# Performance work log

Hardware: AMD Instinct MI355X
Metric: run time of the kernel (lower is better)

Reference implementation:

```python
import jax, jax.numpy as jnp
import numpy as np

N = 20000      # nodes
E = 320000     # edges
IN = 128       # in_channels
HID = 64       # hidden_channels (per-head out dim, concat=False -> mean over heads)
HEADS = 4
NEG_SLOPE = 0.2


def setup_inputs() -> dict:
    key = jax.random.key(0)
    ks = jax.random.split(key, 18)
    g = lambda i, shape: jax.random.normal(ks[i], shape, dtype=jnp.float32) * 0.05
    return {
        "x": jax.random.normal(ks[0], (N, IN), dtype=jnp.float32),
        "edge_index": jax.random.randint(ks[1], (2, E), 0, N),
        # GATConv params: lin weight (no bias in PyG lin), att_src/att_dst, out bias
        "W0": g(2, (IN, HEADS * HID)),
        "W1": g(3, (HID, HEADS * HID)),
        "W2": g(4, (HID, HEADS * HID)),
        "W3": g(5, (HID, HEADS * HID)),
        "a_src": g(6, (4, HEADS, HID)),
        "a_dst": g(7, (4, HEADS, HID)),
        "gat_b": g(8, (4, HID)),
        # residual projection for layer 0 (in_channels != hidden_channels)
        "res_W": g(9, (IN, HID)),
        "res_b": g(10, (HID,)),
        # edge classifier MLP: 2*HID -> HID -> HID -> 1
        "lin_W0": g(11, (2 * HID, HID)),
        "lin_b0": g(12, (HID,)),
        "lin_W1": g(13, (HID, HID)),
        "lin_b1": g(14, (HID,)),
        "lin_W2": g(15, (HID, 1)),
        "lin_b2": g(16, (1,)),
    }


def gat_conv(x, src, dst, W, asrc, adst, b, n):
    # x: [n, F_in]; src/dst: [E_tot] (self-loops included); W: [F_in, H*C]
    h = (x @ W).reshape(n, HEADS, HID)                     # [n, H, C]
    s_src = (h * asrc).sum(-1)                             # [n, H]
    s_dst = (h * adst).sum(-1)                             # [n, H]
    e = jax.nn.leaky_relu(s_src[src] + s_dst[dst], NEG_SLOPE)  # [E_tot, H]
    # segment softmax over incoming edges of each dst node
    m = jax.ops.segment_max(e, dst, num_segments=n)        # [n, H]
    p = jnp.exp(e - m[dst])
    z = jax.ops.segment_sum(p, dst, num_segments=n)
    alpha = p / z[dst]                                     # [E_tot, H]
    out = jax.ops.segment_sum(alpha[:, :, None] * h[src], dst, num_segments=n)  # [n, H, C]
    return out.mean(axis=1) + b                            # concat=False -> mean over heads


def reference(x, edge_index, W0, W1, W2, W3, a_src, a_dst, gat_b,
              res_W, res_b, lin_W0, lin_b0, lin_W1, lin_b1, lin_W2, lin_b2):
    n = x.shape[0]
    loop = jnp.arange(n)
    src = jnp.concatenate([edge_index[0], loop])  # PyG GATConv adds self-loops
    dst = jnp.concatenate([edge_index[1], loop])
    Ws = [W0, W1, W2, W3]
    h = x
    for i in range(4):
        h_prev = h
        h = gat_conv(h, src, dst, Ws[i], a_src[i], a_dst[i], gat_b[i], n)
        if i == 0:
            h = h + h_prev @ res_W + res_b   # projected residual
        else:
            h = h + h_prev
        h = jax.nn.elu(h)
    row, col = edge_index[0], edge_index[1]
    er = jnp.concatenate([h[row], h[col]], axis=1)        # [E, 2*HID]
    er = jax.nn.relu(er @ lin_W0 + lin_b0)                # shapes differ -> no residual
    er = jax.nn.relu(er @ lin_W1 + lin_b1 + er)           # shapes match -> residual
    logits = er @ lin_W2 + lin_b2                          # [E, 1]
    return logits
```

## Files before the change

### kernel.cpp

```cpp
#include <hip/hip_runtime.h>
#include <hip/hip_bf16.h>

#define NSLOPE 0.2f
#define MAXDEG 64

typedef short bf16x8 __attribute__((ext_vector_type(8)));
typedef float f32x4 __attribute__((ext_vector_type(4)));

__device__ __forceinline__ unsigned short f2b(float f) {
    unsigned u = __float_as_uint(f);
    unsigned r = (u + 0x7FFFu + ((u >> 16) & 1u)) >> 16;
    return (unsigned short)r;
}
__device__ __forceinline__ float b2f_lo(unsigned w) {
    return __uint_as_float(w << 16);
}
__device__ __forceinline__ float b2f_hi(unsigned w) {
    return __uint_as_float(w & 0xFFFF0000u);
}
__device__ __forceinline__ float b2f_s(short s) {
    return __uint_as_float(((unsigned)(unsigned short)s) << 16);
}
__device__ __forceinline__ unsigned packb(float lo, float hi) {
    return ((unsigned)f2b(hi) << 16) | (unsigned)f2b(lo);
}

__global__ __launch_bounds__(256) void fill_pad(const int* __restrict__ ei,
                                                int* __restrict__ deg,
                                                int* __restrict__ csrS,
                                                int* __restrict__ epos, int E) {
    int e = blockIdx.x * 256 + threadIdx.x;
    if (e >= E) return;
    int s = ei[e], d = ei[E + e];
    int pos = atomicAdd(&deg[d], 1);
    if (pos < MAXDEG) {
        int slot = d * MAXDEG + pos;
        csrS[slot] = s;
        epos[e] = slot;
    } else {
        epos[e] = -1;
    }
}

__global__ __launch_bounds__(256) void prep_all(
    const float* __restrict__ W0, const float* __restrict__ W1,
    const float* __restrict__ W2, const float* __restrict__ W3,
    const float* __restrict__ resW, const float* __restrict__ linW0,
    const float* __restrict__ linW1, const float* __restrict__ linB0,
    const float* __restrict__ a_src, const float* __restrict__ a_dst,
    const float* __restrict__ gat_b, const float* __restrict__ res_b,
    short* __restrict__ WtC0e, short* __restrict__ WtC1,
    short* __restrict__ WtC2, short* __restrict__ WtC3,
    short* __restrict__ WtUV, short* __restrict__ WbT,
    float* __restrict__ wsd0, float* __restrict__ wsdL,
    float* __restrict__ bias128, float* __restrict__ gb0res) {
    const int bx = blockIdx.x;
    const int tid = threadIdx.x;
    if (bx == 0) {
        for (int idx = blockIdx.y * 256 + tid; idx < 64 * 640; idx += 256 * 16) {
            int j = idx / 640, k = idx - j * 640;
            float v;
            if (k < 512) {
                int h = k >> 7, kk = k & 127;
                v = W0[kk * 256 + h * 64 + j];
            } else {
                v = resW[(k - 512) * 64 + j];
            }
            WtC0e[idx] = (short)f2b(v);
        }
    } else if (bx <= 3) {
        const float* src = (bx == 1) ? W1 : (bx == 2) ? W2 : W3;
        short* dst = (bx == 1) ? WtC1 : (bx == 2) ? WtC2 : WtC3;
        for (int idx = blockIdx.y * 256 + tid; idx < 64 * 256; idx += 256 * 16) {
            int j = idx >> 8, rem = idx & 255;
            int h = rem >> 6, kk = rem & 63;
            dst[idx] = (short)f2b(src[kk * 256 + h * 64 + j]);
        }
    } else if (bx == 4) {
        if (blockIdx.y) return;
        for (int idx = tid; idx < 64 * 64; idx += 256) {
            int nn = idx >> 6, k = idx & 63;
            WtUV[idx] = (short)f2b(linW0[k * 64 + nn]);
        }
    } else if (bx == 5) {
        if (blockIdx.y) return;
        for (int idx = tid; idx < 64 * 64; idx += 256) {
            int nn = idx >> 6, k = idx & 63;
            WtUV[64 * 64 + idx] = (short)f2b(linW0[(k + 64) * 64 + nn]);
        }
    } else if (bx == 6) {
        if (blockIdx.y) return;
        for (int idx = tid; idx < 64 * 64; idx += 256) {
            int nn = idx >> 6, k = idx & 63;
            WbT[idx] = (short)f2b(linW1[k * 64 + nn]);
        }
    } else if (bx == 7) {
        if (blockIdx.y) return;
        if (tid < 128)
            bias128[tid] = (tid < 64) ? linB0[tid] : 0.f;
        else if (tid < 192)
            gb0res[tid - 128] = gat_b[tid - 128] + res_b[tid - 128];
    } else {
        if (blockIdx.y) return;
        int l = bx - 8;
        const float* W = (l == 0) ? W0 : (l == 1) ? W1 : (l == 2) ? W2 : W3;
        const int K = (l == 0) ? 128 : 64;
        float* dst = (l == 0) ? wsd0 : wsdL + (l - 1) * 64 * 8;
        for (int idx = tid; idx < K * 8; idx += 256) {
            int k = idx >> 3, j = idx & 7, h = j & 3;
            const float* av = ((j < 4) ? a_src : a_dst) + l * 256 + h * 64;
            const float* wr = W + k * 256 + h * 64;
            float s = 0.f;
#pragma unroll 8
            for (int c = 0; c < 64; ++c) s += wr[c] * av[c];
            dst[k * 8 + j] = s;
        }
    }
}

__global__ __launch_bounds__(256) void convert_x_scores(
    const float* __restrict__ x, const float* __restrict__ wsd0,
    unsigned* __restrict__ xb2, float* __restrict__ Ssrc,
    float* __restrict__ Sdst, int n) {
    const int wid = threadIdx.x >> 6;
    const int lane = threadIdx.x & 63;
    const int node = blockIdx.x * 4 + wid;
    if (node >= n) return;
    float2 xv = *(const float2*)&x[(size_t)node * 128 + lane * 2];
    xb2[(size_t)node * 64 + lane] = packb(xv.x, xv.y);
    float pv[8];
    const float* w0 = &wsd0[(lane * 2) * 8];
    const float* w1 = &wsd0[(lane * 2 + 1) * 8];
#pragma unroll
    for (int j = 0; j < 8; ++j) pv[j] = xv.x * w0[j] + xv.y * w1[j];
#pragma unroll
    for (int off = 1; off < 64; off <<= 1) {
#pragma unroll
        for (int j = 0; j < 8; ++j) pv[j] += __shfl_xor(pv[j], off, 64);
    }
    if (lane == 0) {
        *(float4*)&Ssrc[node * 4] = make_float4(pv[0], pv[1], pv[2], pv[3]);
        *(float4*)&Sdst[node * 4] = make_float4(pv[4], pv[5], pv[6], pv[7]);
    }
}

__global__ __launch_bounds__(256) void edge_scores(
    const int* __restrict__ ei, const int* __restrict__ epos,
    const float* __restrict__ Ssrc, const float* __restrict__ Sdst,
    float4* __restrict__ p4, int E) {
    int e = blockIdx.x * 256 + threadIdx.x;
    if (e >= E) return;
    int slot = epos[e];
    if (slot < 0) return;
    int s = ei[e], d = ei[E + e];
    float4 ss = *(const float4*)&Ssrc[s * 4];
    float4 dd = *(const float4*)&Sdst[d * 4];
    float c0 = ss.x + dd.x, c1 = ss.y + dd.y, c2 = ss.z + dd.z,
          c3 = ss.w + dd.w;
    c0 = c0 > 0.f ? c0 : NSLOPE * c0;
    c1 = c1 > 0.f ? c1 : NSLOPE * c1;
    c2 = c2 > 0.f ? c2 : NSLOPE * c2;
    c3 = c3 > 0.f ? c3 : NSLOPE * c3;
    p4[slot] = make_float4(__expf(c0), __expf(c1), __expf(c2), __expf(c3));
}

__global__ __launch_bounds__(256) void gat_gather128(
    const int* __restrict__ csrS, const int* __restrict__ deg,
    const float* __restrict__ Ssrc, const float* __restrict__ Sdst,
    const float4* __restrict__ p4, const unsigned* __restrict__ xin,
    unsigned* __restrict__ aggB, int n) {
    const int wid = threadIdx.x >> 6;
    const int lane = threadIdx.x & 63;
    const int node = blockIdx.x * 4 + wid;
    if (node >= n) return;
    const int dn = min(deg[node], MAXDEG);
    const float4 ss = *(const float4*)&Ssrc[node * 4];
    const float4 sd = *(const float4*)&Sdst[node * 4];
    float c0 = ss.x + sd.x, c1 = ss.y + sd.y, c2 = ss.z + sd.z,
          c3 = ss.w + sd.w;
    c0 = c0 > 0.f ? c0 : NSLOPE * c0;
    c1 = c1 > 0.f ? c1 : NSLOPE * c1;
    c2 = c2 > 0.f ? c2 : NSLOPE * c2;
    c3 = c3 > 0.f ? c3 : NSLOPE * c3;
    float ps0 = __expf(c0), ps1 = __expf(c1), ps2 = __expf(c2),
          ps3 = __expf(c3);
    unsigned own = xin[(size_t)node * 64 + lane];
    float f0o = b2f_lo(own), f1o = b2f_hi(own);
    float u00 = ps0 * f0o, u01 = ps0 * f1o;
    float u10 = ps1 * f0o, u11 = ps1 * f1o;
    float u20 = ps2 * f0o, u21 = ps2 * f1o;
    float u30 = ps3 * f0o, u31 = ps3 * f1o;
    float z0 = ps0, z1 = ps1, z2 = ps2, z3 = ps3;
    const int rbase = node * MAXDEG;
#pragma unroll 4
    for (int p = 0; p < dn; ++p) {
        int sj = csrS[rbase + p];
        float4 pv = p4[rbase + p];
        unsigned fv = xin[(size_t)sj * 64 + lane];
        float f0 = b2f_lo(fv), f1 = b2f_hi(fv);
        u00 += pv.x * f0; u01 += pv.x * f1;
        u10 += pv.y * f0; u11 += pv.y * f1;
        u20 += pv.z * f0; u21 += pv.z * f1;
        u30 += pv.w * f0; u31 += pv.w * f1;
        z0 += pv.x; z1 += pv.y; z2 += pv.z; z3 += pv.w;
    }
    float i0 = 0.25f / z0, i1 = 0.25f / z1, i2 = 0.25f / z2, i3 = 0.25f / z3;
    size_t base = (size_t)node * 320;
    aggB[base + lane] = packb(u00 * i0, u01 * i0);
    aggB[base + 64 + lane] = packb(u10 * i1, u11 * i1);
    aggB[base + 128 + lane] = packb(u20 * i2, u21 * i2);
    aggB[base + 192 + lane] = packb(u30 * i3, u31 * i3);
    aggB[base + 256 + lane] = own;
}

__global__ __launch_bounds__(256) void gat_gather64(
    const int* __restrict__ csrS, const int* __restrict__ deg,
    const float* __restrict__ Ssrc, const float* __restrict__ Sdst,
    const float4* __restrict__ p4, const unsigned* __restrict__ fin,
    unsigned* __restrict__ aggB, int n) {
    const int wid = threadIdx.x >> 6;
    const int lane = threadIdx.x & 63;
    const int half = lane >> 5;
    const int cl = lane & 31;
    const int node = blockIdx.x * 4 + wid;
    if (node >= n) return;
    const int dn = min(deg[node], MAXDEG);
    const float4 ss = *(const float4*)&Ssrc[node * 4];
    const float4 sd = *(const float4*)&Sdst[node * 4];
    float c0 = ss.x + sd.x, c1 = ss.y + sd.y, c2 = ss.z + sd.z,
          c3 = ss.w + sd.w;
    c0 = c0 > 0.f ? c0 : NSLOPE * c0;
    c1 = c1 > 0.f ? c1 : NSLOPE * c1;
    c2 = c2 > 0.f ? c2 : NSLOPE * c2;
    c3 = c3 > 0.f ? c3 : NSLOPE * c3;
    float ps0 = __expf(c0), ps1 = __expf(c1), ps2 = __expf(c2),
          ps3 = __expf(c3);
    unsigned own = fin[(size_t)node * 32 + cl];
    float u00 = 0.f, u01 = 0.f, u10 = 0.f, u11 = 0.f;
    float u20 = 0.f, u21 = 0.f, u30 = 0.f, u31 = 0.f;
    float z0 = 0.f, z1 = 0.f, z2 = 0.f, z3 = 0.f;
    const int rbase = node * MAXDEG;
#pragma unroll 4
    for (int p = half; p < dn; p += 2) {
        int sj = csrS[rbase + p];
        float4 pv = p4[rbase + p];
        unsigned fv = fin[(size_t)sj * 32 + cl];
        float f0 = b2f_lo(fv), f1 = b2f_hi(fv);
        u00 += pv.x * f0; u01 += pv.x * f1;
        u10 += pv.y * f0; u11 += pv.y * f1;
        u20 += pv.z * f0; u21 += pv.z * f1;
        u30 += pv.w * f0; u31 += pv.w * f1;
        z0 += pv.x; z1 += pv.y; z2 += pv.z; z3 += pv.w;
    }
    u00 += __shfl_xor(u00, 32, 64); u01 += __shfl_xor(u01, 32, 64);
    u10 += __shfl_xor(u10, 32, 64); u11 += __shfl_xor(u11, 32, 64);
    u20 += __shfl_xor(u20, 32, 64); u21 += __shfl_xor(u21, 32, 64);
    u30 += __shfl_xor(u30, 32, 64); u31 += __shfl_xor(u31, 32, 64);
    z0 += __shfl_xor(z0, 32, 64); z1 += __shfl_xor(z1, 32, 64);
    z2 += __shfl_xor(z2, 32, 64); z3 += __shfl_xor(z3, 32, 64);
    if (half == 0) {
        float f0o = b2f_lo(own), f1o = b2f_hi(own);
        u00 += ps0 * f0o; u01 += ps0 * f1o;
        u10 += ps1 * f0o; u11 += ps1 * f1o;
        u20 += ps2 * f0o; u21 += ps2 * f1o;
        u30 += ps3 * f0o; u31 += ps3 * f1o;
        z0 += ps0; z1 += ps1; z2 += ps2; z3 += ps3;
        float i0 = 0.25f / z0, i1 = 0.25f / z1;
        float i2 = 0.25f / z2, i3 = 0.25f / z3;
        size_t base = (size_t)node * 128;
        aggB[base + cl] = packb(u00 * i0, u01 * i0);
        aggB[base + 32 + cl] = packb(u10 * i1, u11 * i1);
        aggB[base + 64 + cl] = packb(u20 * i2, u21 * i2);
        aggB[base + 96 + cl] = packb(u30 * i3, u31 * i3);
    }
}

template <int KK, bool SCORES>
__global__ __launch_bounds__(256) void gemm_layer(
    const short* __restrict__ Xb, const short* __restrict__ Wt,
    const float* __restrict__ gbias, const float* __restrict__ resid,
    const float* __restrict__ wsd, float* __restrict__ feat,
    short* __restrict__ featb, float* __restrict__ Ssrc,
    float* __restrict__ Sdst, int n) {
    __shared__ __align__(16) short Xs[64 * 136];
    __shared__ __align__(16) short Ws[64 * 40];
    const int tid = threadIdx.x;
    const int nb = blockIdx.x * 64;
    const int wid = tid >> 6;
    const int lane = tid & 63;
    const int t = lane & 15, quad = lane >> 4;
    f32x4 acc[4];
#pragma unroll
    for (int g = 0; g < 4; ++g) acc[g] = (f32x4){0.f, 0.f, 0.f, 0.f};
#pragma unroll 1
    for (int c0 = 0; c0 < KK / 128; ++c0) {
        __syncthreads();
        for (int idx = tid; idx < 1024; idx += 256) {
            int row = idx >> 4, c = idx & 15;
            uint4 v = make_uint4(0, 0, 0, 0);
            if (nb + row < n)
                v = *(const uint4*)(Xb + (size_t)(nb + row) * KK + c0 * 128 +
                                    c * 8);
            *(uint4*)(Xs + row * 136 + c * 8) = v;
        }
#pragma unroll 1
        for (int kc = 0; kc < 4; ++kc) {
            __syncthreads();
            {
                int row = tid >> 2, c = tid & 3;
                uint4 v = *(const uint4*)(Wt + (size_t)row * KK + c0 * 128 +
                                          kc * 32 + c * 8);
                *(uint4*)(Ws + row * 40 + c * 8) = v;
            }
            __syncthreads();
            bf16x8 a =
                *(const bf16x8*)(Xs + (wid * 16 + t) * 136 + kc * 32 + quad * 8);
#pragma unroll
            for (int g = 0; g < 4; ++g) {
                bf16x8 b = *(const bf16x8*)(Ws + (g * 16 + t) * 40 + quad * 8);
                acc[g] =
                    __builtin_amdgcn_mfma_f32_16x16x32_bf16(a, b, acc[g], 0, 0, 0);
            }
        }
    }
    float bv[4];
#pragma unroll
    for (int g = 0; g < 4; ++g) bv[g] = gbias[g * 16 + t];
    float wsv[4][8];
    if (SCORES) {
#pragma unroll
        for (int g = 0; g < 4; ++g) {
            float4 lo = *(const float4*)&wsd[(g * 16 + t) * 8];
            float4 hi = *(const float4*)&wsd[(g * 16 + t) * 8 + 4];
            wsv[g][0] = lo.x; wsv[g][1] = lo.y; wsv[g][2] = lo.z;
            wsv[g][3] = lo.w; wsv[g][4] = hi.x; wsv[g][5] = hi.y;
            wsv[g][6] = hi.z; wsv[g][7] = hi.w;
        }
    }
#pragma unroll
    for (int r = 0; r < 4; ++r) {
        int node = nb + wid * 16 + quad * 4 + r;
        bool ok = node < n;
        float val[4];
#pragma unroll
        for (int g = 0; g < 4; ++g) {
            float v = acc[g][r] + bv[g];
            if (resid && ok) v += resid[(size_t)node * 64 + g * 16 + t];
            v = v > 0.f ? v : expm1f(v);
            val[g] = v;
            if (ok) {
                feat[(size_t)node * 64 + g * 16 + t] = v;
                featb[(size_t)node * 64 + g * 16 + t] = (short)f2b(v);
            }
        }
        if (SCORES) {
            float pv[8];
#pragma unroll
            for (int j = 0; j < 8; ++j) {
                pv[j] = val[0] * wsv[0][j] + val[1] * wsv[1][j] +
                        val[2] * wsv[2][j] + val[3] * wsv[3][j];
            }
#pragma unroll
            for (int off = 1; off < 16; off <<= 1) {
#pragma unroll
                for (int j = 0; j < 8; ++j) pv[j] += __shfl_xor(pv[j], off, 64);
            }
            if (t == 0 && ok) {
                *(float4*)&Ssrc[node * 4] =
                    make_float4(pv[0], pv[1], pv[2], pv[3]);
                *(float4*)&Sdst[node * 4] =
                    make_float4(pv[4], pv[5], pv[6], pv[7]);
            }
        }
    }
}

__global__ __launch_bounds__(256) void uv_gemm(const short* __restrict__ Xb,
                                               const short* __restrict__ Wt,
                                               const float* __restrict__ bias,
                                               short* __restrict__ OutB,
                                               int n) {
    constexpr int K = 64, NG = 8, NC = 128, XSTR = 72;
    __shared__ __align__(16) short Xs[64 * XSTR];
    __shared__ __align__(16) short Ws[NC * 40];
    const int tid = threadIdx.x;
    const int nb = blockIdx.x * 64;
    for (int idx = tid; idx < 64 * 8; idx += 256) {
        int row = idx >> 3, c = idx & 7;
        uint4 v = make_uint4(0, 0, 0, 0);
        if (nb + row < n)
            v = *(const uint4*)(Xb + (size_t)(nb + row) * K + c * 8);
        *(uint4*)(Xs + row * XSTR + c * 8) = v;
    }
    const int wid = tid >> 6;
    const int lane = tid & 63;
    const int t = lane & 15, quad = lane >> 4;
    f32x4 acc[NG];
#pragma unroll
    for (int g = 0; g < NG; ++g) acc[g] = (f32x4){0.f, 0.f, 0.f, 0.f};
#pragma unroll 1
    for (int kc = 0; kc < 2; ++kc) {
        __syncthreads();
        for (int idx = tid; idx < NC * 4; idx += 256) {
            int row = idx >> 2, c = idx & 3;
            uint4 v = *(const uint4*)(Wt + (size_t)row * K + kc * 32 + c * 8);
            *(uint4*)(Ws + row * 40 + c * 8) = v;
        }
        __syncthreads();
        bf16x8 a =
            *(const bf16x8*)(Xs + (wid * 16 + t) * XSTR + kc * 32 + quad * 8);
#pragma unroll
        for (int g = 0; g < NG; ++g) {
            bf16x8 b = *(const bf16x8*)(Ws + (g * 16 + t) * 40 + quad * 8);
            acc[g] = __builtin_amdgcn_mfma_f32_16x16x32_bf16(a, b, acc[g], 0, 0, 0);
        }
    }
    float bv[NG];
#pragma unroll
    for (int g = 0; g < NG; ++g) bv[g] = bias[g * 16 + t];
#pragma unroll
    for (int r = 0; r < 4; ++r) {
        int node = nb + wid * 16 + quad * 4 + r;
        if (node >= n) continue;
#pragma unroll
        for (int g = 0; g < NG; ++g)
            OutB[(size_t)node * NC + g * 16 + t] = (short)f2b(acc[g][r] + bv[g]);
    }
}

__global__ __launch_bounds__(256) void edge_mlp3(
    const int* __restrict__ ei, const unsigned* __restrict__ UV,
    const short* __restrict__ WbT, const float* __restrict__ bb,
    const float* __restrict__ Wc, const float* __restrict__ bc,
    float* __restrict__ out, int E) {
    __shared__ __align__(16) short t1b[64 * 72];
    __shared__ __align__(16) short wbs[64 * 72];
    const int tid = threadIdx.x;
    const int eBase = blockIdx.x * 64;
    for (int idx = tid; idx < 512; idx += 256) {
        int row = idx >> 3, c = idx & 7;
        *(uint4*)(wbs + row * 72 + c * 8) =
            *(const uint4*)(WbT + row * 64 + c * 8);
    }
    {
        const int j = tid & 31;
        const int eg = tid >> 5;
        int rr[8], cc[8];
#pragma unroll
        for (int it = 0; it < 8; ++it) {
            int e = eBase + it * 8 + eg;
            rr[it] = (e < E) ? ei[e] : 0;
            cc[it] = (e < E) ? ei[E + e] : 0;
        }
#pragma unroll
        for (int it = 0; it < 8; ++it) {
            unsigned uu = UV[(size_t)rr[it] * 64 + j];
            unsigned vv = UV[(size_t)cc[it] * 64 + 32 + j];
            float lo = fmaxf(b2f_lo(uu) + b2f_lo(vv), 0.f);
            float hi = fmaxf(b2f_hi(uu) + b2f_hi(vv), 0.f);
            *(unsigned*)(t1b + (it * 8 + eg) * 72 + j * 2) = packb(lo, hi);
        }
    }
    __syncthreads();
    const int w = tid >> 6, lane = tid & 63;
    const int t = lane & 15, quad = lane >> 4;
    f32x4 acc[4];
#pragma unroll
    for (int g = 0; g < 4; ++g) acc[g] = (f32x4){0.f, 0.f, 0.f, 0.f};
#pragma unroll
    for (int kc = 0; kc < 2; ++kc) {
        bf16x8 a = *(const bf16x8*)(t1b + (w * 16 + t) * 72 + kc * 32 + quad * 8);
#pragma unroll
        for (int g = 0; g < 4; ++g) {
            bf16x8 b = *(const bf16x8*)(wbs + (g * 16 + t) * 72 + kc * 32 + quad * 8);
            acc[g] = __builtin_amdgcn_mfma_f32_16x16x32_bf16(a, b, acc[g], 0, 0, 0);
        }
    }
    float wcv[4], bbv[4];
#pragma unroll
    for (int g = 0; g < 4; ++g) {
        wcv[g] = Wc[g * 16 + t];
        bbv[g] = bb[g * 16 + t];
    }
    const float bcv = bc[0];
#pragma unroll
    for (int r = 0; r < 4; ++r) {
        int el = w * 16 + quad * 4 + r;
        float part = 0.f;
#pragma unroll
        for (int g = 0; g < 4; ++g) {
            float t1v = b2f_s(t1b[el * 72 + g * 16 + t]);
            float t2 = fmaxf(acc[g][r] + bbv[g] + t1v, 0.f);
            part += t2 * wcv[g];
        }
        part += __shfl_xor(part, 1, 64);
        part += __shfl_xor(part, 2, 64);
        part += __shfl_xor(part, 4, 64);
        part += __shfl_xor(part, 8, 64);
        int e = eBase + el;
        if (t == 0 && e < E) out[e] = part + bcv;
    }
}

extern "C" void kernel_launch(void* const* d_in, const int* in_sizes, int n_in,
                              void* d_out, int out_size, void* d_ws,
                              size_t ws_size, hipStream_t stream) {
    const float* x = (const float*)d_in[0];
    const int* ei = (const int*)d_in[1];
    const float* W0 = (const float*)d_in[2];
    const float* W1 = (const float*)d_in[3];
    const float* W2 = (const float*)d_in[4];
    const float* W3 = (const float*)d_in[5];
    const float* a_src = (const float*)d_in[6];
    const float* a_dst = (const float*)d_in[7];
    const float* gat_b = (const float*)d_in[8];
    const float* res_W = (const float*)d_in[9];
    const float* res_b = (const float*)d_in[10];
    const float* lin_W0 = (const float*)d_in[11];
    const float* lin_b0 = (const float*)d_in[12];
    const float* lin_W1 = (const float*)d_in[13];
    const float* lin_b1 = (const float*)d_in[14];
    const float* lin_W2 = (const float*)d_in[15];
    const float* lin_b2 = (const float*)d_in[16];
    float* out = (float*)d_out;

    const int N = in_sizes[0] / 128;
    const int E = in_sizes[1] / 2;

    char* ws = (char*)d_ws;
    float4* p4 = (float4*)ws;
    unsigned* aggB = (unsigned*)(p4 + (size_t)N * 64);
    float* featA = (float*)(aggB + (size_t)N * 320);
    float* featB = featA + (size_t)N * 64;
    unsigned* xb2 = (unsigned*)(featB + (size_t)N * 64);
    unsigned* featbA = xb2 + (size_t)N * 64;
    unsigned* featbB = featbA + (size_t)N * 32;
    float* Ssrc = (float*)(featbB + (size_t)N * 32);
    float* Sdst = Ssrc + (size_t)N * 4;
    short* WtC0e = (short*)(Sdst + (size_t)N * 4);
    short* WtC1 = WtC0e + 64 * 640;
    short* WtC2 = WtC1 + 64 * 256;
    short* WtC3 = WtC2 + 64 * 256;
    short* WtUV = WtC3 + 64 * 256;
    short* WbT = WtUV + 128 * 64;
    float* wsd0 = (float*)(WbT + 64 * 64);
    float* wsdL = wsd0 + 128 * 8;
    float* bias128 = wsdL + 3 * 64 * 8;
    float* gb0res = bias128 + 128;
    int* deg = (int*)(gb0res + 64);
    int* csrS = deg + N;
    int* epos = csrS + (size_t)N * MAXDEG;
    unsigned* UVb = aggB;

    const int gemmBlocks = (N + 63) / 64;
    const int eBlocks = (E + 255) / 256;
    const int nodeW = (N + 3) / 4;

    hipMemsetAsync(deg, 0, (size_t)N * sizeof(int), stream);
    fill_pad<<<eBlocks, 256, 0, stream>>>(ei, deg, csrS, epos, E);

    prep_all<<<dim3(12, 16), 256, 0, stream>>>(
        W0, W1, W2, W3, res_W, lin_W0, lin_W1, lin_b0, a_src, a_dst, gat_b,
        res_b, WtC0e, WtC1, WtC2, WtC3, WtUV, WbT, wsd0, wsdL, bias128,
        gb0res);
    convert_x_scores<<<nodeW, 256, 0, stream>>>(x, wsd0, xb2, Ssrc, Sdst, N);

    edge_scores<<<eBlocks, 256, 0, stream>>>(ei, epos, Ssrc, Sdst, p4, E);
    gat_gather128<<<nodeW, 256, 0, stream>>>(csrS, deg, Ssrc, Sdst, p4, xb2,
                                             aggB, N);
    gemm_layer<640, true><<<gemmBlocks, 256, 0, stream>>>(
        (const short*)aggB, WtC0e, gb0res, nullptr, wsdL, featA,
        (short*)featbA, Ssrc, Sdst, N);

    const short* WtCs[3] = {WtC1, WtC2, WtC3};
    float* feats[4] = {featA, featB, featA, featB};
    unsigned* featbs[4] = {featbA, featbB, featbA, featbB};
    for (int i = 1; i < 4; ++i) {
        edge_scores<<<eBlocks, 256, 0, stream>>>(ei, epos, Ssrc, Sdst, p4, E);
        gat_gather64<<<nodeW, 256, 0, stream>>>(csrS, deg, Ssrc, Sdst, p4,
                                                featbs[i - 1], aggB, N);
        if (i < 3)
            gemm_layer<256, true><<<gemmBlocks, 256, 0, stream>>>(
                (const short*)aggB, WtCs[i - 1], gat_b + i * 64, feats[i - 1],
                wsdL + i * 64 * 8, feats[i], (short*)featbs[i], Ssrc, Sdst, N);
        else
            gemm_layer<256, false><<<gemmBlocks, 256, 0, stream>>>(
                (const short*)aggB, WtCs[i - 1], gat_b + i * 64, feats[i - 1],
                nullptr, feats[i], (short*)featbs[i], Ssrc, Sdst, N);
    }

    uv_gemm<<<gemmBlocks, 256, 0, stream>>>((const short*)featbB, WtUV,
                                            bias128, (short*)UVb, N);
    edge_mlp3<<<(E + 63) / 64, 256, 0, stream>>>(ei, UVb, WbT, lin_b1, lin_W2,
                                                 lin_b2, out, E);
}
```

Baseline: 337.5 us.

## Fuse edge scores into gathers, merge last GAT layer with UV GEMM

Removes the per-layer edge_scores kernel and the padded p4 buffer. The gather kernels now recompute leaky-relu and exp from Ssrc of each neighbour inline, trading a float4 p4 read for a float4 Ssrc gather plus four exps per edge. The last GAT GEMM is fused with the UV projection GEMM, so the layer-3 output never round-trips through global memory. The deg memset is folded into prep_all, which drops one launch, and the epos array is eliminated.

```diff
diff --git a/kernel.cpp b/kernel.cpp
--- a/kernel.cpp
+++ b/kernel.cpp
@@ -27,19 +27,12 @@
 
 __global__ __launch_bounds__(256) void fill_pad(const int* __restrict__ ei,
                                                 int* __restrict__ deg,
-                                                int* __restrict__ csrS,
-                                                int* __restrict__ epos, int E) {
+                                                int* __restrict__ csrS, int E) {
     int e = blockIdx.x * 256 + threadIdx.x;
     if (e >= E) return;
     int s = ei[e], d = ei[E + e];
     int pos = atomicAdd(&deg[d], 1);
-    if (pos < MAXDEG) {
-        int slot = d * MAXDEG + pos;
-        csrS[slot] = s;
-        epos[e] = slot;
-    } else {
-        epos[e] = -1;
-    }
+    if (pos < MAXDEG) csrS[d * MAXDEG + pos] = s;
 }
 
 __global__ __launch_bounds__(256) void prep_all(
@@ -53,7 +46,8 @@
     short* __restrict__ WtC2, short* __restrict__ WtC3,
     short* __restrict__ WtUV, short* __restrict__ WbT,
     float* __restrict__ wsd0, float* __restrict__ wsdL,
-    float* __restrict__ bias128, float* __restrict__ gb0res) {
+    float* __restrict__ bias128, float* __restrict__ gb0res,
+    int* __restrict__ deg, int n) {
     const int bx = blockIdx.x;
     const int tid = threadIdx.x;
     if (bx == 0) {
@@ -100,7 +94,7 @@
             bias128[tid] = (tid < 64) ? linB0[tid] : 0.f;
         else if (tid < 192)
             gb0res[tid - 128] = gat_b[tid - 128] + res_b[tid - 128];
-    } else {
+    } else if (bx <= 11) {
         if (blockIdx.y) return;
         int l = bx - 8;
         const float* W = (l == 0) ? W0 : (l == 1) ? W1 : (l == 2) ? W2 : W3;
@@ -115,6 +109,8 @@
             for (int c = 0; c < 64; ++c) s += wr[c] * av[c];
             dst[k * 8 + j] = s;
         }
+    } else {
+        for (int i = blockIdx.y * 256 + tid; i < n; i += 256 * 16) deg[i] = 0;
     }
 }
 
@@ -144,38 +140,17 @@
     }
 }
 
-__global__ __launch_bounds__(256) void edge_scores(
-    const int* __restrict__ ei, const int* __restrict__ epos,
-    const float* __restrict__ Ssrc, const float* __restrict__ Sdst,
-    float4* __restrict__ p4, int E) {
-    int e = blockIdx.x * 256 + threadIdx.x;
-    if (e >= E) return;
-    int slot = epos[e];
-    if (slot < 0) return;
-    int s = ei[e], d = ei[E + e];
-    float4 ss = *(const float4*)&Ssrc[s * 4];
-    float4 dd = *(const float4*)&Sdst[d * 4];
-    float c0 = ss.x + dd.x, c1 = ss.y + dd.y, c2 = ss.z + dd.z,
-          c3 = ss.w + dd.w;
-    c0 = c0 > 0.f ? c0 : NSLOPE * c0;
-    c1 = c1 > 0.f ? c1 : NSLOPE * c1;
-    c2 = c2 > 0.f ? c2 : NSLOPE * c2;
-    c3 = c3 > 0.f ? c3 : NSLOPE * c3;
-    p4[slot] = make_float4(__expf(c0), __expf(c1), __expf(c2), __expf(c3));
-}
-
 __global__ __launch_bounds__(256) void gat_gather128(
     const int* __restrict__ csrS, const int* __restrict__ deg,
     const float* __restrict__ Ssrc, const float* __restrict__ Sdst,
-    const float4* __restrict__ p4, const unsigned* __restrict__ xin,
-    unsigned* __restrict__ aggB, int n) {
+    const unsigned* __restrict__ xin, unsigned* __restrict__ aggB, int n) {
     const int wid = threadIdx.x >> 6;
     const int lane = threadIdx.x & 63;
     const int node = blockIdx.x * 4 + wid;
     if (node >= n) return;
     const int dn = min(deg[node], MAXDEG);
+    const float4 sd = *(const float4*)&Sdst[node * 4];
     const float4 ss = *(const float4*)&Ssrc[node * 4];
-    const float4 sd = *(const float4*)&Sdst[node * 4];
     float c0 = ss.x + sd.x, c1 = ss.y + sd.y, c2 = ss.z + sd.z,
           c3 = ss.w + sd.w;
     c0 = c0 > 0.f ? c0 : NSLOPE * c0;
@@ -195,14 +170,22 @@
 #pragma unroll 4
     for (int p = 0; p < dn; ++p) {
         int sj = csrS[rbase + p];
-        float4 pv = p4[rbase + p];
+        float4 sv = *(const float4*)&Ssrc[sj * 4];
         unsigned fv = xin[(size_t)sj * 64 + lane];
+        float e0 = sv.x + sd.x, e1 = sv.y + sd.y;
+        float e2 = sv.z + sd.z, e3 = sv.w + sd.w;
+        e0 = e0 > 0.f ? e0 : NSLOPE * e0;
+        e1 = e1 > 0.f ? e1 : NSLOPE * e1;
+        e2 = e2 > 0.f ? e2 : NSLOPE * e2;
+        e3 = e3 > 0.f ? e3 : NSLOPE * e3;
+        float p0 = __expf(e0), p1 = __expf(e1);
+        float p2 = __expf(e2), p3 = __expf(e3);
         float f0 = b2f_lo(fv), f1 = b2f_hi(fv);
-        u00 += pv.x * f0; u01 += pv.x * f1;
-        u10 += pv.y * f0; u11 += pv.y * f1;
-        u20 += pv.z * f0; u21 += pv.z * f1;
-        u30 += pv.w * f0; u31 += pv.w * f1;
-        z0 += pv.x; z1 += pv.y; z2 += pv.z; z3 += pv.w;
+        u00 += p0 * f0; u01 += p0 * f1;
+        u10 += p1 * f0; u11 += p1 * f1;
+        u20 += p2 * f0; u21 += p2 * f1;
+        u30 += p3 * f0; u31 += p3 * f1;
+        z0 += p0; z1 += p1; z2 += p2; z3 += p3;
     }
     float i0 = 0.25f / z0, i1 = 0.25f / z1, i2 = 0.25f / z2, i3 = 0.25f / z3;
     size_t base = (size_t)node * 320;
@@ -216,8 +199,7 @@
 __global__ __launch_bounds__(256) void gat_gather64(
     const int* __restrict__ csrS, const int* __restrict__ deg,
     const float* __restrict__ Ssrc, const float* __restrict__ Sdst,
-    const float4* __restrict__ p4, const unsigned* __restrict__ fin,
-    unsigned* __restrict__ aggB, int n) {
+    const unsigned* __restrict__ fin, unsigned* __restrict__ aggB, int n) {
     const int wid = threadIdx.x >> 6;
     const int lane = threadIdx.x & 63;
     const int half = lane >> 5;
@@ -225,8 +207,8 @@
     const int node = blockIdx.x * 4 + wid;
     if (node >= n) return;
     const int dn = min(deg[node], MAXDEG);
+    const float4 sd = *(const float4*)&Sdst[node * 4];
     const float4 ss = *(const float4*)&Ssrc[node * 4];
-    const float4 sd = *(const float4*)&Sdst[node * 4];
     float c0 = ss.x + sd.x, c1 = ss.y + sd.y, c2 = ss.z + sd.z,
           c3 = ss.w + sd.w;
     c0 = c0 > 0.f ? c0 : NSLOPE * c0;
@@ -243,14 +225,22 @@
 #pragma unroll 4
     for (int p = half; p < dn; p += 2) {
         int sj = csrS[rbase + p];
-        float4 pv = p4[rbase + p];
+        float4 sv = *(const float4*)&Ssrc[sj * 4];
         unsigned fv = fin[(size_t)sj * 32 + cl];
+        float e0 = sv.x + sd.x, e1 = sv.y + sd.y;
+        float e2 = sv.z + sd.z, e3 = sv.w + sd.w;
+        e0 = e0 > 0.f ? e0 : NSLOPE * e0;
+        e1 = e1 > 0.f ? e1 : NSLOPE * e1;
+        e2 = e2 > 0.f ? e2 : NSLOPE * e2;
+        e3 = e3 > 0.f ? e3 : NSLOPE * e3;
+        float p0 = __expf(e0), p1 = __expf(e1);
+        float p2 = __expf(e2), p3 = __expf(e3);
         float f0 = b2f_lo(fv), f1 = b2f_hi(fv);
-        u00 += pv.x * f0; u01 += pv.x * f1;
-        u10 += pv.y * f0; u11 += pv.y * f1;
-        u20 += pv.z * f0; u21 += pv.z * f1;
-        u30 += pv.w * f0; u31 += pv.w * f1;
-        z0 += pv.x; z1 += pv.y; z2 += pv.z; z3 += pv.w;
+        u00 += p0 * f0; u01 += p0 * f1;
+        u10 += p1 * f0; u11 += p1 * f1;
+        u20 += p2 * f0; u21 += p2 * f1;
+        u30 += p3 * f0; u31 += p3 * f1;
+        z0 += p0; z1 += p1; z2 += p2; z3 += p3;
     }
     u00 += __shfl_xor(u00, 32, 64); u01 += __shfl_xor(u01, 32, 64);
     u10 += __shfl_xor(u10, 32, 64); u11 += __shfl_xor(u11, 32, 64);
@@ -375,56 +365,100 @@
     }
 }
 
-__global__ __launch_bounds__(256) void uv_gemm(const short* __restrict__ Xb,
-                                               const short* __restrict__ Wt,
-                                               const float* __restrict__ bias,
-                                               short* __restrict__ OutB,
-                                               int n) {
-    constexpr int K = 64, NG = 8, NC = 128, XSTR = 72;
-    __shared__ __align__(16) short Xs[64 * XSTR];
-    __shared__ __align__(16) short Ws[NC * 40];
+__global__ __launch_bounds__(256) void gemm_layer_uv(
+    const short* __restrict__ Xb, const short* __restrict__ Wt,
+    const float* __restrict__ gbias, const float* __restrict__ resid,
+    const short* __restrict__ WtUV, const float* __restrict__ bias128,
+    short* __restrict__ OutUV, int n) {
+    constexpr int KK = 256;
+    __shared__ __align__(16) short Xs[64 * 136];
+    __shared__ __align__(16) short Ws[128 * 40];
     const int tid = threadIdx.x;
     const int nb = blockIdx.x * 64;
-    for (int idx = tid; idx < 64 * 8; idx += 256) {
-        int row = idx >> 3, c = idx & 7;
-        uint4 v = make_uint4(0, 0, 0, 0);
-        if (nb + row < n)
-            v = *(const uint4*)(Xb + (size_t)(nb + row) * K + c * 8);
-        *(uint4*)(Xs + row * XSTR + c * 8) = v;
-    }
     const int wid = tid >> 6;
     const int lane = tid & 63;
     const int t = lane & 15, quad = lane >> 4;
-    f32x4 acc[NG];
-#pragma unroll
-    for (int g = 0; g < NG; ++g) acc[g] = (f32x4){0.f, 0.f, 0.f, 0.f};
+    f32x4 acc[4];
+#pragma unroll
+    for (int g = 0; g < 4; ++g) acc[g] = (f32x4){0.f, 0.f, 0.f, 0.f};
+#pragma unroll 1
+    for (int c0 = 0; c0 < KK / 128; ++c0) {
+        __syncthreads();
+        for (int idx = tid; idx < 1024; idx += 256) {
+            int row = idx >> 4, c = idx & 15;
+            uint4 v = make_uint4(0, 0, 0, 0);
+            if (nb + row < n)
+                v = *(const uint4*)(Xb + (size_t)(nb + row) * KK + c0 * 128 +
+                                    c * 8);
+            *(uint4*)(Xs + row * 136 + c * 8) = v;
+        }
+#pragma unroll 1
+        for (int kc = 0; kc < 4; ++kc) {
+            __syncthreads();
+            {
+                int row = tid >> 2, c = tid & 3;
+                uint4 v = *(const uint4*)(Wt + (size_t)row * KK + c0 * 128 +
+                                          kc * 32 + c * 8);
+                *(uint4*)(Ws + row * 40 + c * 8) = v;
+            }
+            __syncthreads();
+            bf16x8 a =
+                *(const bf16x8*)(Xs + (wid * 16 + t) * 136 + kc * 32 + quad * 8);
+#pragma unroll
+            for (int g = 0; g < 4; ++g) {
+                bf16x8 b = *(const bf16x8*)(Ws + (g * 16 + t) * 40 + quad * 8);
+                acc[g] =
+                    __builtin_amdgcn_mfma_f32_16x16x32_bf16(a, b, acc[g], 0, 0, 0);
+            }
+        }
+    }
+    float bv[4];
+#pragma unroll
+    for (int g = 0; g < 4; ++g) bv[g] = gbias[g * 16 + t];
+    __syncthreads();
+#pragma unroll
+    for (int r = 0; r < 4; ++r) {
+        int node = nb + wid * 16 + quad * 4 + r;
+        bool ok = node < n;
+        int lrow = wid * 16 + quad * 4 + r;
+#pragma unroll
+        for (int g = 0; g < 4; ++g) {
+            float v = acc[g][r] + bv[g];
+            if (ok) v += resid[(size_t)node * 64 + g * 16 + t];
+            v = v > 0.f ? v : expm1f(v);
+            Xs[lrow * 72 + g * 16 + t] = (short)f2b(v);
+        }
+    }
+    f32x4 acc2[8];
+#pragma unroll
+    for (int g = 0; g < 8; ++g) acc2[g] = (f32x4){0.f, 0.f, 0.f, 0.f};
 #pragma unroll 1
     for (int kc = 0; kc < 2; ++kc) {
         __syncthreads();
-        for (int idx = tid; idx < NC * 4; idx += 256) {
+        for (int idx = tid; idx < 512; idx += 256) {
             int row = idx >> 2, c = idx & 3;
-            uint4 v = *(const uint4*)(Wt + (size_t)row * K + kc * 32 + c * 8);
+            uint4 v = *(const uint4*)(WtUV + (size_t)row * 64 + kc * 32 + c * 8);
             *(uint4*)(Ws + row * 40 + c * 8) = v;
         }
         __syncthreads();
-        bf16x8 a =
-            *(const bf16x8*)(Xs + (wid * 16 + t) * XSTR + kc * 32 + quad * 8);
-#pragma unroll
-        for (int g = 0; g < NG; ++g) {
+        bf16x8 a = *(const bf16x8*)(Xs + (wid * 16 + t) * 72 + kc * 32 + quad * 8);
+#pragma unroll
+        for (int g = 0; g < 8; ++g) {
             bf16x8 b = *(const bf16x8*)(Ws + (g * 16 + t) * 40 + quad * 8);
-            acc[g] = __builtin_amdgcn_mfma_f32_16x16x32_bf16(a, b, acc[g], 0, 0, 0);
-        }
-    }
-    float bv[NG];
-#pragma unroll
-    for (int g = 0; g < NG; ++g) bv[g] = bias[g * 16 + t];
+            acc2[g] = __builtin_amdgcn_mfma_f32_16x16x32_bf16(a, b, acc2[g], 0, 0, 0);
+        }
+    }
+    float b2[8];
+#pragma unroll
+    for (int g = 0; g < 8; ++g) b2[g] = bias128[g * 16 + t];
 #pragma unroll
     for (int r = 0; r < 4; ++r) {
         int node = nb + wid * 16 + quad * 4 + r;
         if (node >= n) continue;
 #pragma unroll
-        for (int g = 0; g < NG; ++g)
-            OutB[(size_t)node * NC + g * 16 + t] = (short)f2b(acc[g][r] + bv[g]);
+        for (int g = 0; g < 8; ++g)
+            OutUV[(size_t)node * 128 + g * 16 + t] =
+                (short)f2b(acc2[g][r] + b2[g]);
     }
 }
 
@@ -528,14 +562,14 @@
     const int E = in_sizes[1] / 2;
 
     char* ws = (char*)d_ws;
-    float4* p4 = (float4*)ws;
-    unsigned* aggB = (unsigned*)(p4 + (size_t)N * 64);
+    unsigned* aggB = (unsigned*)ws;
     float* featA = (float*)(aggB + (size_t)N * 320);
     float* featB = featA + (size_t)N * 64;
     unsigned* xb2 = (unsigned*)(featB + (size_t)N * 64);
     unsigned* featbA = xb2 + (size_t)N * 64;
     unsigned* featbB = featbA + (size_t)N * 32;
-    float* Ssrc = (float*)(featbB + (size_t)N * 32);
+    unsigned* UVb = featbB + (size_t)N * 32;
+    float* Ssrc = (float*)(UVb + (size_t)N * 64);
     float* Sdst = Ssrc + (size_t)N * 4;
     short* WtC0e = (short*)(Sdst + (size_t)N * 4);
     short* WtC1 = WtC0e + 64 * 640;
@@ -549,48 +583,41 @@
     float* gb0res = bias128 + 128;
     int* deg = (int*)(gb0res + 64);
     int* csrS = deg + N;
-    int* epos = csrS + (size_t)N * MAXDEG;
-    unsigned* UVb = aggB;
 
     const int gemmBlocks = (N + 63) / 64;
     const int eBlocks = (E + 255) / 256;
     const int nodeW = (N + 3) / 4;
 
-    hipMemsetAsync(deg, 0, (size_t)N * sizeof(int), stream);
-    fill_pad<<<eBlocks, 256, 0, stream>>>(ei, deg, csrS, epos, E);
-
-    prep_all<<<dim3(12, 16), 256, 0, stream>>>(
+    prep_all<<<dim3(13, 16), 256, 0, stream>>>(
         W0, W1, W2, W3, res_W, lin_W0, lin_W1, lin_b0, a_src, a_dst, gat_b,
         res_b, WtC0e, WtC1, WtC2, WtC3, WtUV, WbT, wsd0, wsdL, bias128,
-        gb0res);
+        gb0res, deg, N);
+    fill_pad<<<eBlocks, 256, 0, stream>>>(ei, deg, csrS, E);
     convert_x_scores<<<nodeW, 256, 0, stream>>>(x, wsd0, xb2, Ssrc, Sdst, N);
 
-    edge_scores<<<eBlocks, 256, 0, stream>>>(ei, epos, Ssrc, Sdst, p4, E);
-    gat_gather128<<<nodeW, 256, 0, stream>>>(csrS, deg, Ssrc, Sdst, p4, xb2,
-                                             aggB, N);
+    gat_gather128<<<nodeW, 256, 0, stream>>>(csrS, deg, Ssrc, Sdst, xb2, aggB,
+                                             N);
     gemm_layer<640, true><<<gemmBlocks, 256, 0, stream>>>(
         (const short*)aggB, WtC0e, gb0res, nullptr, wsdL, featA,
         (short*)featbA, Ssrc, Sdst, N);
 
-    const short* WtCs[3] = {WtC1, WtC2, WtC3};
-    float* feats[4] = {featA, featB, featA, featB};
-    unsigned* featbs[4] = {featbA, featbB, featbA, featbB};
-    for (int i = 1; i < 4; ++i) {
-        edge_scores<<<eBlocks, 256, 0, stream>>>(ei, epos, Ssrc, Sdst, p4, E);
-        gat_gather64<<<nodeW, 256, 0, stream>>>(csrS, deg, Ssrc, Sdst, p4,
-                                                featbs[i - 1], aggB, N);
-        if (i < 3)
-            gemm_layer<256, true><<<gemmBlocks, 256, 0, stream>>>(
-                (const short*)aggB, WtCs[i - 1], gat_b + i * 64, feats[i - 1],
-                wsdL + i * 64 * 8, feats[i], (short*)featbs[i], Ssrc, Sdst, N);
-        else
-            gemm_layer<256, false><<<gemmBlocks, 256, 0, stream>>>(
-                (const short*)aggB, WtCs[i - 1], gat_b + i * 64, feats[i - 1],
-                nullptr, feats[i], (short*)featbs[i], Ssrc, Sdst, N);
-    }
-
-    uv_gemm<<<gemmBlocks, 256, 0, stream>>>((const short*)featbB, WtUV,
-                                            bias128, (short*)UVb, N);
+    gat_gather64<<<nodeW, 256, 0, stream>>>(csrS, deg, Ssrc, Sdst, featbA,
+                                            aggB, N);
+    gemm_layer<256, true><<<gemmBlocks, 256, 0, stream>>>(
+        (const short*)aggB, WtC1, gat_b + 64, featA, wsdL + 64 * 8, featB,
+        (short*)featbB, Ssrc, Sdst, N);
+    gat_gather64<<<nodeW, 256, 0, stream>>>(csrS, deg, Ssrc, Sdst, featbB,
+                                            aggB, N);
+    gemm_layer<256, true><<<gemmBlocks, 256, 0, stream>>>(
+        (const short*)aggB, WtC2, gat_b + 128, featB, wsdL + 2 * 64 * 8,
+        featA, (short*)featbA, Ssrc, Sdst, N);
+
+    gat_gather64<<<nodeW, 256, 0, stream>>>(csrS, deg, Ssrc, Sdst, featbA,
+                                            aggB, N);
+    gemm_layer_uv<<<gemmBlocks, 256, 0, stream>>>(
+        (const short*)aggB, WtC3, gat_b + 192, featA, WtUV, bias128,
+        (short*)UVb, N);
+
     edge_mlp3<<<(E + 63) / 64, 256, 0, stream>>>(ei, UVb, WbT, lin_b1, lin_W2,
                                                  lin_b2, out, E);
 }
```

Measured after the change: 326.3 us. 1.03x faster.
